# Optimization experiments

Measured on AMD Instinct MI355X. Metric: run time of the kernel, lower is better.

## Reference

```python
import jax, jax.numpy as jnp
import numpy as np

B, S, D, H = 2, 2048, 1024, 16
HD = D // H  # head_dim = 64


def setup_inputs() -> dict:
    key = jax.random.key(0)
    ks = jax.random.split(key, 10)
    std = 1.0 / np.sqrt(D)
    inputs = jax.random.normal(ks[0], (B, S, D), dtype=jnp.float32)
    # stacked per-head projection weights: [H, HD, D] (row-major like nn.Linear)
    Wq = jax.random.uniform(ks[1], (H, HD, D), jnp.float32, -std, std)
    bq = jax.random.uniform(ks[2], (H, HD), jnp.float32, -std, std)
    Wk = jax.random.uniform(ks[3], (H, HD, D), jnp.float32, -std, std)
    bk = jax.random.uniform(ks[4], (H, HD), jnp.float32, -std, std)
    Wv = jax.random.uniform(ks[5], (H, HD, D), jnp.float32, -std, std)
    bv = jax.random.uniform(ks[6], (H, HD), jnp.float32, -std, std)
    Wo = jax.random.uniform(ks[7], (D, D), jnp.float32, -std, std)
    bo = jax.random.uniform(ks[8], (D,), jnp.float32, -std, std)
    return {"inputs": inputs, "Wq": Wq, "bq": bq, "Wk": Wk, "bk": bk,
            "Wv": Wv, "bv": bv, "Wo": Wo, "bo": bo}


def reference(inputs, Wq, bq, Wk, bk, Wv, bv, Wo, bo):
    # per-head projections, batched over heads: [B,H,S,HD]
    q = jnp.einsum('bsd,hed->bhse', inputs, Wq) + bq[None, :, None, :]
    k = jnp.einsum('bsd,hed->bhse', inputs, Wk) + bk[None, :, None, :]
    v = jnp.einsum('bsd,hed->bhse', inputs, Wv) + bv[None, :, None, :]
    scale = 1.0 / np.sqrt(HD).astype(np.float32)
    # explicit [B,H,S,S] score matrix, as in the original naive attention
    scores = jnp.einsum('bhqe,bhke->bhqk', q, k) * scale
    causal = jnp.tril(jnp.ones((S, S), dtype=bool))
    scores = jnp.where(causal[None, None], scores, jnp.float32(-jnp.inf))
    attn = jax.nn.softmax(scores, axis=-1)  # dropout p=0 -> identity
    wv = jnp.einsum('bhqk,bhke->bhqe', attn, v)
    # concat heads along feature dim: [B,S,H*HD] = [B,S,D]
    z = wv.transpose(0, 2, 1, 3).reshape(B, S, D)
    out = jnp.einsum('bsd,ed->bse', z, Wo) + bo
    return out
```

## Files before the change

### kernel.cpp

```cpp
#include <hip/hip_runtime.h>
#include <math.h>

#define Bx 2
#define Sx 2048
#define Dx 1024
#define Hx 16
#define HDx 64
#define Mx (Bx*Sx)

typedef __bf16 bf16x8 __attribute__((ext_vector_type(8)));
typedef __bf16 bf16x4 __attribute__((ext_vector_type(4)));
typedef float  f32x4  __attribute__((ext_vector_type(4)));

#define SCL 0.18033688011112042f

__device__ __forceinline__ void gload_lds16(const __bf16* g, __bf16* l) {
  __builtin_amdgcn_global_load_lds(
      (const __attribute__((address_space(1))) unsigned int*)g,
      (__attribute__((address_space(3))) unsigned int*)l, 16, 0, 0);
}

__device__ __forceinline__ void cvt8(const float* s, __bf16* d) {
  float4 a = *(const float4*)s;
  float4 b = *(const float4*)(s + 4);
  bf16x8 o;
  o[0] = (__bf16)a.x; o[1] = (__bf16)a.y; o[2] = (__bf16)a.z; o[3] = (__bf16)a.w;
  o[4] = (__bf16)b.x; o[5] = (__bf16)b.y; o[6] = (__bf16)b.z; o[7] = (__bf16)b.w;
  *(bf16x8*)d = o;
}

__global__ __launch_bounds__(256) void cvt_kernel(
    const float* __restrict__ x, const float* __restrict__ Wq,
    const float* __restrict__ Wk, const float* __restrict__ Wv,
    const float* __restrict__ Wo, const float* __restrict__ bq,
    const float* __restrict__ bk, const float* __restrict__ bv,
    __bf16* __restrict__ xb, __bf16* __restrict__ wqkv,
    __bf16* __restrict__ wob, float* __restrict__ bqkv)
{
  const int bid = blockIdx.x;
  const int t = threadIdx.x;
  const size_t MEG = 1024u * 1024u;
  if (bid < 2048) {
    size_t e = (size_t)bid * 2048 + t * 8;
    cvt8(x + e, xb + e);
  } else if (bid < 3584) {
    size_t e = (size_t)(bid - 2048) * 2048 + t * 8;
    const float* src = (e < MEG) ? (Wq + e) : (e < 2 * MEG) ? (Wk + (e - MEG)) : (Wv + (e - 2 * MEG));
    cvt8(src, wqkv + e);
  } else if (bid < 4096) {
    size_t e = (size_t)(bid - 3584) * 2048 + t * 8;
    cvt8(Wo + e, wob + e);
  } else {
    for (int i = t; i < 3072; i += 256)
      bqkv[i] = (i < 1024) ? bq[i] : (i < 2048) ? bk[i - 1024] : bv[i - 2048];
  }
}

template<int TM, int TN, int MODE>
__global__ __launch_bounds__(256) void gemm_k(
    const __bf16* __restrict__ A, const __bf16* __restrict__ W,
    const float* __restrict__ bias, float* __restrict__ Cf,
    __bf16* __restrict__ Cb, __bf16* __restrict__ vT,
    int M, int N, int K, int ldc)
{
  __shared__ __align__(16) char smem[35840];
  __bf16* As = (__bf16*)smem;
  __bf16* Bs = (__bf16*)(smem + (size_t)TM * 64 * 2);

  constexpr int MS = TM / 32;
  constexpr int NS = TN / 32;
  const int tid = threadIdx.x;
  const int lane = tid & 63, wave = tid >> 6;
  const int l16 = lane & 15, quad = lane >> 4;
  const int wm = (wave >> 1) * (TM / 2);
  const int wn = (wave & 1) * (TN / 2);
  const int m0 = blockIdx.y * TM;
  const int n0 = blockIdx.x * TN;
  const int swz = l16 & 7;

  const f32x4 zero = {0.f, 0.f, 0.f, 0.f};
  f32x4 acc[MS][NS];
#pragma unroll
  for (int i = 0; i < MS; ++i)
#pragma unroll
    for (int j = 0; j < NS; ++j) acc[i][j] = zero;

  const int srow = tid >> 3;
  const int scs = (tid & 7) ^ (srow & 7);
  const __bf16* Ag = A + (size_t)(m0 + srow) * K + scs * 8;
  const __bf16* Wg = W + (size_t)(n0 + srow) * K + scs * 8;

  for (int k0 = 0; k0 < K; k0 += 64) {
    __syncthreads();
#pragma unroll
    for (int i = 0; i < TM / 32; ++i)
      gload_lds16(Ag + (size_t)(i * 32) * K + k0, &As[(i * 256 + tid) * 8]);
#pragma unroll
    for (int i = 0; i < TN / 32; ++i)
      gload_lds16(Wg + (size_t)(i * 32) * K + k0, &Bs[(i * 256 + tid) * 8]);
    __syncthreads();

#pragma unroll
    for (int hk = 0; hk < 2; ++hk) {
      const int ph = ((hk * 4 + quad) ^ swz) * 8;
      bf16x8 af[MS], bfr[NS];
#pragma unroll
      for (int i = 0; i < MS; ++i)
        af[i] = *(const bf16x8*)&As[(wm + i * 16 + l16) * 64 + ph];
#pragma unroll
      for (int j = 0; j < NS; ++j)
        bfr[j] = *(const bf16x8*)&Bs[(wn + j * 16 + l16) * 64 + ph];
#pragma unroll
      for (int i = 0; i < MS; ++i)
#pragma unroll
        for (int j = 0; j < NS; ++j)
          acc[i][j] = __builtin_amdgcn_mfma_f32_16x16x32_bf16(af[i], bfr[j], acc[i][j], 0, 0, 0);
    }
  }

  __syncthreads();
  if (MODE == 0) {
    float* Cs = (float*)smem;
    constexpr int cst = TN + 4;
#pragma unroll
    for (int j = 0; j < NS; ++j) {
      const int c = wn + j * 16 + l16;
      const float bv_ = bias[n0 + c];
#pragma unroll
      for (int i = 0; i < MS; ++i) {
        const int r0 = wm + i * 16 + quad * 4;
#pragma unroll
        for (int g = 0; g < 4; ++g)
          Cs[(r0 + g) * cst + c] = acc[i][j][g] + bv_;
      }
    }
    __syncthreads();
    constexpr int passes = TM * TN / (256 * 4);
#pragma unroll
    for (int p = 0; p < passes; ++p) {
      const int slot = p * 256 + tid;
      const int row = slot / (TN / 4);
      const int col4 = (slot % (TN / 4)) * 4;
      f32x4 v = *(const f32x4*)&Cs[row * cst + col4];
      *(f32x4*)&Cf[(size_t)(m0 + row) * ldc + n0 + col4] = v;
    }
  } else {
    __bf16* Cs = (__bf16*)smem;
    constexpr int cst = TN + 8;
    const bool vtile = (n0 >= 2048);
    if (!vtile) {
#pragma unroll
      for (int j = 0; j < NS; ++j) {
        const int c = wn + j * 16 + l16;
        const float bv_ = bias[n0 + c];
        const float sc = ((n0 + c) < 1024) ? SCL : 1.0f;
#pragma unroll
        for (int i = 0; i < MS; ++i) {
          const int r0 = wm + i * 16 + quad * 4;
#pragma unroll
          for (int g = 0; g < 4; ++g)
            Cs[(r0 + g) * cst + c] = (__bf16)((acc[i][j][g] + bv_) * sc);
        }
      }
      __syncthreads();
      constexpr int passes = TM * TN / (256 * 8);
#pragma unroll
      for (int p = 0; p < passes; ++p) {
        const int slot = p * 256 + tid;
        const int row = slot / (TN / 8);
        const int col8 = (slot % (TN / 8)) * 8;
        bf16x8 v = *(const bf16x8*)&Cs[row * cst + col8];
        *(bf16x8*)&Cb[(size_t)(m0 + row) * 3072 + n0 + col8] = v;
      }
    } else {
      constexpr int cstT = TM + 8;
#pragma unroll
      for (int j = 0; j < NS; ++j) {
        const int c = wn + j * 16 + l16;
        const float bv_ = bias[n0 + c];
#pragma unroll
        for (int i = 0; i < MS; ++i) {
          const int r0 = wm + i * 16 + quad * 4;
#pragma unroll
          for (int g = 0; g < 4; ++g)
            Cs[c * cstT + r0 + g] = (__bf16)(acc[i][j][g] + bv_);
        }
      }
      __syncthreads();
      const int bb = m0 >> 11, ml = m0 & 2047;
      constexpr int passes = TM * TN / (256 * 8);
#pragma unroll
      for (int p = 0; p < passes; ++p) {
        const int slot = p * 256 + tid;
        const int dd = slot / (TM / 8);
        const int ss8 = (slot % (TM / 8)) * 8;
        bf16x8 v = *(const bf16x8*)&Cs[dd * cstT + ss8];
        const int c2 = n0 - 2048 + dd;
        const int hh = c2 >> 6, ddd = c2 & 63;
        *(bf16x8*)&vT[((size_t)(bb * 16 + hh) * 64 + ddd) * 2048 + ml + ss8] = v;
      }
    }
  }
}

__global__ __launch_bounds__(256) void attn_mfma(
    const __bf16* __restrict__ qkv, const __bf16* __restrict__ vT,
    __bf16* __restrict__ zb)
{
  __shared__ __bf16 Qs[64 * 64];
  __shared__ __bf16 Ks[2][64 * 64];
  __shared__ __bf16 Vs[3][64 * 64];

  const int tid = threadIdx.x;
  const int lane = tid & 63, wave = tid >> 6;
  const int l16 = lane & 15, quad = lane >> 4;
  const int bx = blockIdx.x;
  const int qt = 31 - (bx >> 5);
  const int bh = bx & 31;
  const int h = bh & 15, b = bh >> 4;
  const int q0 = qt * 64;

  const __bf16* qg = qkv + (size_t)b * 2048 * 3072 + h * 64;
  const __bf16* kg = qg + 1024;
  const __bf16* vg = vT + (size_t)bh * 64 * 2048;

#define STAGE_KV(kt_, kbuf, vbuf)                                               \
  { const int kn = (kt_) * 64;                                                  \
    _Pragma("unroll")                                                           \
    for (int i = 0; i < 2; ++i) {                                               \
      int slot = i * 256 + tid;                                                 \
      int row = slot >> 3, ph2 = slot & 7;                                      \
      int cs = ph2 ^ (row & 7);                                                 \
      gload_lds16(kg + (size_t)(kn + row) * 3072 + cs * 8, &Ks[kbuf][slot * 8]);\
      gload_lds16(vg + (size_t)row * 2048 + kn + cs * 8, &Vs[vbuf][slot * 8]);  \
    } }

#pragma unroll
  for (int i = 0; i < 2; ++i) {
    int slot = i * 256 + tid;
    int row = slot >> 3, ph2 = slot & 7;
    int cs = ph2 ^ (row & 7);
    gload_lds16(qg + (size_t)(q0 + row) * 3072 + cs * 8, &Qs[slot * 8]);
  }
  STAGE_KV(0, 0, 0)
  __syncthreads();

  const int sw0 = ((quad) ^ (l16 & 7)) * 8;
  const int sw1 = ((quad + 4) ^ (l16 & 7)) * 8;
  const int mrow = wave * 16 + l16;

  bf16x8 qf0 = *(const bf16x8*)&Qs[mrow * 64 + sw0];
  bf16x8 qf1 = *(const bf16x8*)&Qs[mrow * 64 + sw1];
  __bf16* P = &Qs[wave * 16 * 64];

  bf16x8 onesf;
  {
    __bf16 ov = (l16 == 0) ? (__bf16)1.0f : (__bf16)0.0f;
#pragma unroll
    for (int i = 0; i < 8; ++i) onesf[i] = ov;
  }

  const f32x4 zero = {0.f, 0.f, 0.f, 0.f};
  f32x4 O[4], Ol = zero;
#pragma unroll
  for (int j = 0; j < 4; ++j) O[j] = zero;
  f32x4 s_cur[4], s_next[4];

#define S_TILE(sdst, kb)                                                        \
  { _Pragma("unroll")                                                           \
    for (int j = 0; j < 4; ++j) sdst[j] = zero;                                 \
    _Pragma("unroll")                                                           \
    for (int j = 0; j < 4; ++j) {                                               \
      bf16x8 kf0 = *(const bf16x8*)&Ks[kb][(j * 16 + l16) * 64 + sw0];          \
      sdst[j] = __builtin_amdgcn_mfma_f32_16x16x32_bf16(qf0, kf0, sdst[j],0,0,0);\
      bf16x8 kf1 = *(const bf16x8*)&Ks[kb][(j * 16 + l16) * 64 + sw1];          \
      sdst[j] = __builtin_amdgcn_mfma_f32_16x16x32_bf16(qf1, kf1, sdst[j],0,0,0);\
    } }

#define EXP_P(s, DIAG)                                                          \
  { _Pragma("unroll")                                                           \
    for (int j = 0; j < 4; ++j) {                                               \
      _Pragma("unroll")                                                         \
      for (int g = 0; g < 4; ++g) {                                             \
        float p = __builtin_exp2f(s[j][g]);                                     \
        if (DIAG && (j * 16 + l16) > (wave * 16 + quad * 4 + g)) p = 0.f;       \
        s[j][g] = p;                                                            \
      }                                                                         \
    }                                                                           \
    _Pragma("unroll")                                                           \
    for (int j = 0; j < 4; ++j) {                                               \
      const int col = j * 16 + l16;                                             \
      const int ch = col >> 3, cin = col & 7;                                   \
      _Pragma("unroll")                                                         \
      for (int g = 0; g < 4; ++g) {                                             \
        const int row = quad * 4 + g;                                           \
        P[row * 64 + ((ch ^ (row & 7)) * 8) + cin] = (__bf16)s[j][g];           \
      }                                                                         \
    } }

#define PV_TILE(vb)                                                             \
  { bf16x8 pf0 = *(const bf16x8*)&P[l16 * 64 + sw0];                            \
    bf16x8 pf1 = *(const bf16x8*)&P[l16 * 64 + sw1];                            \
    _Pragma("unroll")                                                           \
    for (int j = 0; j < 4; ++j) {                                               \
      bf16x8 vf0 = *(const bf16x8*)&Vs[vb][(j * 16 + l16) * 64 + sw0];          \
      O[j] = __builtin_amdgcn_mfma_f32_16x16x32_bf16(pf0, vf0, O[j], 0, 0, 0);  \
      bf16x8 vf1 = *(const bf16x8*)&Vs[vb][(j * 16 + l16) * 64 + sw1];          \
      O[j] = __builtin_amdgcn_mfma_f32_16x16x32_bf16(pf1, vf1, O[j], 0, 0, 0);  \
    }                                                                           \
    Ol = __builtin_amdgcn_mfma_f32_16x16x32_bf16(pf0, onesf, Ol, 0, 0, 0);      \
    Ol = __builtin_amdgcn_mfma_f32_16x16x32_bf16(pf1, onesf, Ol, 0, 0, 0); }

  if (qt > 0) STAGE_KV(1, 1, 1)
  S_TILE(s_cur, 0)
  if (qt > 0) __syncthreads();

  for (int t = 0; t < qt; ++t) {
    EXP_P(s_cur, false)
    S_TILE(s_next, (t + 1) & 1)
    PV_TILE(t % 3)
    if (t + 2 <= qt) STAGE_KV(t + 2, t & 1, (t + 2) % 3)
    __syncthreads();
#pragma unroll
    for (int j = 0; j < 4; ++j) s_cur[j] = s_next[j];
  }
  EXP_P(s_cur, true)
  PV_TILE(qt % 3)

  const int rq = q0 + wave * 16 + quad * 4;
#pragma unroll
  for (int g = 0; g < 4; ++g) {
    const float lv = __shfl(Ol[g], quad * 16);
    const float inv = 1.0f / lv;
    const size_t rb = (size_t)(b * 2048 + rq + g) * 1024 + h * 64 + l16;
#pragma unroll
    for (int j = 0; j < 4; ++j)
      zb[rb + j * 16] = (__bf16)(O[j][g] * inv);
  }
}

extern "C" void kernel_launch(void* const* d_in, const int* in_sizes, int n_in,
                              void* d_out, int out_size, void* d_ws, size_t ws_size,
                              hipStream_t stream) {
  (void)in_sizes; (void)n_in; (void)out_size; (void)ws_size;
  const float* x  = (const float*)d_in[0];
  const float* Wq = (const float*)d_in[1];
  const float* bq = (const float*)d_in[2];
  const float* Wk = (const float*)d_in[3];
  const float* bk = (const float*)d_in[4];
  const float* Wv = (const float*)d_in[5];
  const float* bv = (const float*)d_in[6];
  const float* Wo = (const float*)d_in[7];
  const float* bo = (const float*)d_in[8];

  char* ws = (char*)d_ws;
  __bf16* xb   = (__bf16*)(ws);
  __bf16* wqkv = (__bf16*)(ws + (8ull  << 20));
  __bf16* wob  = (__bf16*)(ws + (14ull << 20));
  float*  bqkv = (float*) (ws + (16ull << 20));
  __bf16* qkv  = (__bf16*)(ws + (17ull << 20));
  __bf16* vT   = (__bf16*)(ws + (41ull << 20));
  __bf16* zb   = (__bf16*)(ws + (49ull << 20));

  cvt_kernel<<<4097, 256, 0, stream>>>(x, Wq, Wk, Wv, Wo, bq, bk, bv,
                                       xb, wqkv, wob, bqkv);
  gemm_k<128, 128, 1><<<dim3(24, 32), 256, 0, stream>>>(
      xb, wqkv, bqkv, nullptr, qkv, vT, Mx, 3072, 1024, 0);
  attn_mfma<<<1024, 256, 0, stream>>>(qkv, vT, zb);
  gemm_k<128, 64, 0><<<dim3(16, 32), 256, 0, stream>>>(
      zb, wob, bo, (float*)d_out, nullptr, nullptr, Mx, 1024, 1024, 1024);
}
```

Measured before the change: 194.3 us.

## Use 128-row query tiles with split-K for long causal tiles plus combine kernel

The attention kernel now processes 128 query rows per block (two 16-row sub-tiles per wave), which reuses each K/V tile across twice as many queries. The 8 longest query tiles of each head are split in half along the key dimension to balance work across blocks. Their partial outputs are written as fp16 with fp32 row sums, and a new combine kernel merges them. This adds an extra launch and partial-result traffic, reduces V buffering from three to two stages, and sets a 3-block occupancy hint.

```diff
diff --git a/kernel.cpp b/kernel.cpp
--- a/kernel.cpp
+++ b/kernel.cpp
@@ -11,6 +11,7 @@
 typedef __bf16 bf16x8 __attribute__((ext_vector_type(8)));
 typedef __bf16 bf16x4 __attribute__((ext_vector_type(4)));
 typedef float  f32x4  __attribute__((ext_vector_type(4)));
+typedef _Float16 f16x8 __attribute__((ext_vector_type(8)));
 
 #define SCL 0.18033688011112042f
 
@@ -203,55 +204,72 @@
   }
 }
 
-__global__ __launch_bounds__(256) void attn_mfma(
+__global__ __launch_bounds__(256, 3) void attn_mfma(
     const __bf16* __restrict__ qkv, const __bf16* __restrict__ vT,
-    __bf16* __restrict__ zb)
+    __bf16* __restrict__ zb, _Float16* __restrict__ Ph, float* __restrict__ Pl)
 {
-  __shared__ __bf16 Qs[64 * 64];
+  __shared__ __bf16 Qs[128 * 64];
   __shared__ __bf16 Ks[2][64 * 64];
-  __shared__ __bf16 Vs[3][64 * 64];
+  __shared__ __bf16 Vs[2][64 * 64];
 
   const int tid = threadIdx.x;
   const int lane = tid & 63, wave = tid >> 6;
   const int l16 = lane & 15, quad = lane >> 4;
+  const int swz = l16 & 7;
   const int bx = blockIdx.x;
-  const int qt = 31 - (bx >> 5);
   const int bh = bx & 31;
+  const int g = bx >> 5;
+  int qt, half, split;
+  if (g < 16) { split = 1; qt = 15 - (g >> 1); half = g & 1; }
+  else        { split = 0; qt = g - 16; half = 0; }
+  const int q0 = qt * 128;
+  const int nk = 2 * qt + 2;
+  const int t0 = (split && half) ? (qt + 1) : 0;
+  const int t1 = (split && !half) ? (qt + 1) : nk;
+  const int nt = t1 - t0;
   const int h = bh & 15, b = bh >> 4;
-  const int q0 = qt * 64;
 
   const __bf16* qg = qkv + (size_t)b * 2048 * 3072 + h * 64;
   const __bf16* kg = qg + 1024;
   const __bf16* vg = vT + (size_t)bh * 64 * 2048;
 
-#define STAGE_KV(kt_, kbuf, vbuf)                                               \
+#define STAGE_K8(kt_, kb)                                                       \
   { const int kn = (kt_) * 64;                                                  \
     _Pragma("unroll")                                                           \
     for (int i = 0; i < 2; ++i) {                                               \
       int slot = i * 256 + tid;                                                 \
-      int row = slot >> 3, ph2 = slot & 7;                                      \
-      int cs = ph2 ^ (row & 7);                                                 \
-      gload_lds16(kg + (size_t)(kn + row) * 3072 + cs * 8, &Ks[kbuf][slot * 8]);\
-      gload_lds16(vg + (size_t)row * 2048 + kn + cs * 8, &Vs[vbuf][slot * 8]);  \
+      int row = slot >> 3;                                                      \
+      int cs = (slot & 7) ^ (row & 7);                                          \
+      gload_lds16(kg + (size_t)(kn + row) * 3072 + cs * 8, &Ks[kb][slot * 8]);  \
     } }
-
-#pragma unroll
-  for (int i = 0; i < 2; ++i) {
+#define STAGE_V8(kt_, vb)                                                       \
+  { const int kn = (kt_) * 64;                                                  \
+    _Pragma("unroll")                                                           \
+    for (int i = 0; i < 2; ++i) {                                               \
+      int slot = i * 256 + tid;                                                 \
+      int row = slot >> 3;                                                      \
+      int cs = (slot & 7) ^ (row & 7);                                          \
+      gload_lds16(vg + (size_t)row * 2048 + kn + cs * 8, &Vs[vb][slot * 8]);    \
+    } }
+
+#pragma unroll
+  for (int i = 0; i < 4; ++i) {
     int slot = i * 256 + tid;
-    int row = slot >> 3, ph2 = slot & 7;
-    int cs = ph2 ^ (row & 7);
+    int row = slot >> 3;
+    int cs = (slot & 7) ^ (row & 7);
     gload_lds16(qg + (size_t)(q0 + row) * 3072 + cs * 8, &Qs[slot * 8]);
   }
-  STAGE_KV(0, 0, 0)
+  STAGE_K8(t0, 0)
+  STAGE_V8(t0, 0)
   __syncthreads();
 
-  const int sw0 = ((quad) ^ (l16 & 7)) * 8;
-  const int sw1 = ((quad + 4) ^ (l16 & 7)) * 8;
-  const int mrow = wave * 16 + l16;
-
-  bf16x8 qf0 = *(const bf16x8*)&Qs[mrow * 64 + sw0];
-  bf16x8 qf1 = *(const bf16x8*)&Qs[mrow * 64 + sw1];
-  __bf16* P = &Qs[wave * 16 * 64];
+  bf16x8 qf[2][2];
+#pragma unroll
+  for (int s = 0; s < 2; ++s)
+#pragma unroll
+    for (int kk = 0; kk < 2; ++kk)
+      qf[s][kk] = *(const bf16x8*)&Qs[(wave * 32 + s * 16 + l16) * 64 + ((kk * 4 + quad) ^ swz) * 8];
+  __bf16* P = &Qs[wave * 32 * 64];
 
   bf16x8 onesf;
   {
@@ -261,81 +279,136 @@
   }
 
   const f32x4 zero = {0.f, 0.f, 0.f, 0.f};
-  f32x4 O[4], Ol = zero;
-#pragma unroll
-  for (int j = 0; j < 4; ++j) O[j] = zero;
-  f32x4 s_cur[4], s_next[4];
-
-#define S_TILE(sdst, kb)                                                        \
-  { _Pragma("unroll")                                                           \
-    for (int j = 0; j < 4; ++j) sdst[j] = zero;                                 \
-    _Pragma("unroll")                                                           \
-    for (int j = 0; j < 4; ++j) {                                               \
-      bf16x8 kf0 = *(const bf16x8*)&Ks[kb][(j * 16 + l16) * 64 + sw0];          \
-      sdst[j] = __builtin_amdgcn_mfma_f32_16x16x32_bf16(qf0, kf0, sdst[j],0,0,0);\
-      bf16x8 kf1 = *(const bf16x8*)&Ks[kb][(j * 16 + l16) * 64 + sw1];          \
-      sdst[j] = __builtin_amdgcn_mfma_f32_16x16x32_bf16(qf1, kf1, sdst[j],0,0,0);\
-    } }
-
-#define EXP_P(s, DIAG)                                                          \
-  { _Pragma("unroll")                                                           \
-    for (int j = 0; j < 4; ++j) {                                               \
-      _Pragma("unroll")                                                         \
-      for (int g = 0; g < 4; ++g) {                                             \
-        float p = __builtin_exp2f(s[j][g]);                                     \
-        if (DIAG && (j * 16 + l16) > (wave * 16 + quad * 4 + g)) p = 0.f;       \
-        s[j][g] = p;                                                            \
-      }                                                                         \
-    }                                                                           \
-    _Pragma("unroll")                                                           \
-    for (int j = 0; j < 4; ++j) {                                               \
-      const int col = j * 16 + l16;                                             \
-      const int ch = col >> 3, cin = col & 7;                                   \
-      _Pragma("unroll")                                                         \
-      for (int g = 0; g < 4; ++g) {                                             \
-        const int row = quad * 4 + g;                                           \
-        P[row * 64 + ((ch ^ (row & 7)) * 8) + cin] = (__bf16)s[j][g];           \
-      }                                                                         \
-    } }
-
-#define PV_TILE(vb)                                                             \
-  { bf16x8 pf0 = *(const bf16x8*)&P[l16 * 64 + sw0];                            \
-    bf16x8 pf1 = *(const bf16x8*)&P[l16 * 64 + sw1];                            \
-    _Pragma("unroll")                                                           \
-    for (int j = 0; j < 4; ++j) {                                               \
-      bf16x8 vf0 = *(const bf16x8*)&Vs[vb][(j * 16 + l16) * 64 + sw0];          \
-      O[j] = __builtin_amdgcn_mfma_f32_16x16x32_bf16(pf0, vf0, O[j], 0, 0, 0);  \
-      bf16x8 vf1 = *(const bf16x8*)&Vs[vb][(j * 16 + l16) * 64 + sw1];          \
-      O[j] = __builtin_amdgcn_mfma_f32_16x16x32_bf16(pf1, vf1, O[j], 0, 0, 0);  \
-    }                                                                           \
-    Ol = __builtin_amdgcn_mfma_f32_16x16x32_bf16(pf0, onesf, Ol, 0, 0, 0);      \
-    Ol = __builtin_amdgcn_mfma_f32_16x16x32_bf16(pf1, onesf, Ol, 0, 0, 0); }
-
-  if (qt > 0) STAGE_KV(1, 1, 1)
-  S_TILE(s_cur, 0)
-  if (qt > 0) __syncthreads();
-
-  for (int t = 0; t < qt; ++t) {
-    EXP_P(s_cur, false)
-    S_TILE(s_next, (t + 1) & 1)
-    PV_TILE(t % 3)
-    if (t + 2 <= qt) STAGE_KV(t + 2, t & 1, (t + 2) % 3)
-    __syncthreads();
-#pragma unroll
-    for (int j = 0; j < 4; ++j) s_cur[j] = s_next[j];
-  }
-  EXP_P(s_cur, true)
-  PV_TILE(qt % 3)
-
-  const int rq = q0 + wave * 16 + quad * 4;
-#pragma unroll
-  for (int g = 0; g < 4; ++g) {
-    const float lv = __shfl(Ol[g], quad * 16);
-    const float inv = 1.0f / lv;
-    const size_t rb = (size_t)(b * 2048 + rq + g) * 1024 + h * 64 + l16;
-#pragma unroll
-    for (int j = 0; j < 4; ++j)
-      zb[rb + j * 16] = (__bf16)(O[j][g] * inv);
+  f32x4 O[2][4], Ol[2];
+#pragma unroll
+  for (int s = 0; s < 2; ++s) {
+    Ol[s] = zero;
+#pragma unroll
+    for (int j = 0; j < 4; ++j) O[s][j] = zero;
+  }
+
+  for (int u = 0; u < nt; ++u) {
+    const int kt = t0 + u;
+    const int kb = u & 1;
+    if (u + 1 < nt) {
+      STAGE_K8(kt + 1, kb ^ 1)
+      STAGE_V8(kt + 1, kb ^ 1)
+    }
+    f32x4 sv[2][4];
+#pragma unroll
+    for (int s = 0; s < 2; ++s)
+#pragma unroll
+      for (int j = 0; j < 4; ++j) sv[s][j] = zero;
+#pragma unroll
+    for (int kk = 0; kk < 2; ++kk) {
+      const int ph = ((kk * 4 + quad) ^ swz) * 8;
+#pragma unroll
+      for (int j = 0; j < 4; ++j) {
+        bf16x8 kf = *(const bf16x8*)&Ks[kb][(j * 16 + l16) * 64 + ph];
+        sv[0][j] = __builtin_amdgcn_mfma_f32_16x16x32_bf16(qf[0][kk], kf, sv[0][j], 0, 0, 0);
+        sv[1][j] = __builtin_amdgcn_mfma_f32_16x16x32_bf16(qf[1][kk], kf, sv[1][j], 0, 0, 0);
+      }
+    }
+    const bool md = (kt >= 2 * qt);
+#pragma unroll
+    for (int s = 0; s < 2; ++s)
+#pragma unroll
+      for (int j = 0; j < 4; ++j) {
+        const int cg = kt * 64 + j * 16 + l16;
+        const int rg = q0 + wave * 32 + s * 16 + quad * 4;
+#pragma unroll
+        for (int gg = 0; gg < 4; ++gg) {
+          float p = __builtin_exp2f(sv[s][j][gg]);
+          if (md && cg > rg + gg) p = 0.f;
+          sv[s][j][gg] = p;
+        }
+      }
+#pragma unroll
+    for (int s = 0; s < 2; ++s)
+#pragma unroll
+      for (int j = 0; j < 4; ++j) {
+        const int col = j * 16 + l16;
+        const int ch = col >> 3, cin = col & 7;
+#pragma unroll
+        for (int gg = 0; gg < 4; ++gg) {
+          const int rl = s * 16 + quad * 4 + gg;
+          P[rl * 64 + ((ch ^ (rl & 7)) * 8) + cin] = (__bf16)sv[s][j][gg];
+        }
+      }
+#pragma unroll
+    for (int kk = 0; kk < 2; ++kk) {
+      const int ph = ((kk * 4 + quad) ^ swz) * 8;
+      bf16x8 pf0 = *(const bf16x8*)&P[l16 * 64 + ph];
+      bf16x8 pf1 = *(const bf16x8*)&P[(16 + l16) * 64 + ph];
+#pragma unroll
+      for (int j = 0; j < 4; ++j) {
+        bf16x8 vf = *(const bf16x8*)&Vs[kb][(j * 16 + l16) * 64 + ph];
+        O[0][j] = __builtin_amdgcn_mfma_f32_16x16x32_bf16(pf0, vf, O[0][j], 0, 0, 0);
+        O[1][j] = __builtin_amdgcn_mfma_f32_16x16x32_bf16(pf1, vf, O[1][j], 0, 0, 0);
+      }
+      Ol[0] = __builtin_amdgcn_mfma_f32_16x16x32_bf16(pf0, onesf, Ol[0], 0, 0, 0);
+      Ol[1] = __builtin_amdgcn_mfma_f32_16x16x32_bf16(pf1, onesf, Ol[1], 0, 0, 0);
+    }
+    if (u + 1 < nt) __syncthreads();
+  }
+
+  if (!split) {
+#pragma unroll
+    for (int s = 0; s < 2; ++s)
+#pragma unroll
+      for (int gg = 0; gg < 4; ++gg) {
+        const float lv = __shfl(Ol[s][gg], quad * 16);
+        const float inv = 1.0f / lv;
+        const int rq = q0 + wave * 32 + s * 16 + quad * 4 + gg;
+        const size_t rb = (size_t)(b * 2048 + rq) * 1024 + h * 64 + l16;
+#pragma unroll
+        for (int j = 0; j < 4; ++j)
+          zb[rb + j * 16] = (__bf16)(O[s][j][gg] * inv);
+      }
+  } else {
+    const int p2 = ((bh << 3) + (qt - 8)) * 2 + half;
+    _Float16* Op = Ph + (size_t)p2 * 8192;
+    float* Lp = Pl + (size_t)p2 * 128;
+#pragma unroll
+    for (int s = 0; s < 2; ++s)
+#pragma unroll
+      for (int gg = 0; gg < 4; ++gg) {
+        const int rl = wave * 32 + s * 16 + quad * 4 + gg;
+#pragma unroll
+        for (int j = 0; j < 4; ++j)
+          Op[rl * 64 + j * 16 + l16] = (_Float16)O[s][j][gg];
+        if (l16 == 0) Lp[rl] = Ol[s][gg];
+      }
+  }
+}
+
+__global__ __launch_bounds__(256) void combine_kernel(
+    const _Float16* __restrict__ Ph, const float* __restrict__ Pl,
+    __bf16* __restrict__ zb)
+{
+  const int bxx = blockIdx.x;
+  const int st = bxx >> 1, sub = bxx & 1;
+  const int bh = st >> 3, qi = st & 7;
+  const int qt = 8 + qi;
+  const int b = bh >> 4, h = bh & 15;
+  const int p0 = st * 2;
+  const _Float16* O0 = Ph + (size_t)p0 * 8192;
+  const _Float16* O1 = O0 + 8192;
+  const float* L0 = Pl + (size_t)p0 * 128;
+  const float* L1 = L0 + 128;
+  const int r = sub * 64 + (threadIdx.x >> 2);
+  const int c0 = (threadIdx.x & 3) * 16;
+  const float inv = 1.0f / (L0[r] + L1[r]);
+  const size_t base = (size_t)(b * 2048 + qt * 128 + r) * 1024 + h * 64 + c0;
+#pragma unroll
+  for (int u = 0; u < 2; ++u) {
+    f16x8 a = *(const f16x8*)&O0[r * 64 + c0 + u * 8];
+    f16x8 c = *(const f16x8*)&O1[r * 64 + c0 + u * 8];
+    bf16x8 o;
+#pragma unroll
+    for (int i = 0; i < 8; ++i)
+      o[i] = (__bf16)(((float)a[i] + (float)c[i]) * inv);
+    *(bf16x8*)&zb[base + u * 8] = o;
   }
 }
 
@@ -361,12 +434,15 @@
   __bf16* qkv  = (__bf16*)(ws + (17ull << 20));
   __bf16* vT   = (__bf16*)(ws + (41ull << 20));
   __bf16* zb   = (__bf16*)(ws + (49ull << 20));
+  _Float16* Ph = (_Float16*)(ws);
+  float*    Pl = (float*)(ws + (8ull << 20) + (512ull << 10));
 
   cvt_kernel<<<4097, 256, 0, stream>>>(x, Wq, Wk, Wv, Wo, bq, bk, bv,
                                        xb, wqkv, wob, bqkv);
   gemm_k<128, 128, 1><<<dim3(24, 32), 256, 0, stream>>>(
       xb, wqkv, bqkv, nullptr, qkv, vT, Mx, 3072, 1024, 0);
-  attn_mfma<<<1024, 256, 0, stream>>>(qkv, vT, zb);
+  attn_mfma<<<768, 256, 0, stream>>>(qkv, vT, zb, Ph, Pl);
+  combine_kernel<<<512, 256, 0, stream>>>(Ph, Pl, zb);
   gemm_k<128, 64, 0><<<dim3(16, 32), 256, 0, stream>>>(
       zb, wob, bo, (float*)d_out, nullptr, nullptr, Mx, 1024, 1024, 1024);
 }
```

New measurement: 205.6 us. 5.8% more time.
